# Optimization experiments

Hardware: AMD Instinct MI355X
Metric: run time of the kernel (lower is better)

Reference implementation:

```python
import jax, jax.numpy as jnp
import numpy as np

D = 4  # search range -> 2*D+1 = 9 correlation channels


def setup_inputs() -> dict:
    key = jax.random.key(0)
    k1, k2 = jax.random.split(key)
    N, C, H, W = 4, 128, 192, 640
    feature1 = jax.random.normal(k1, (N, C, H, W), dtype=jnp.float32)
    feature2 = jax.random.normal(k2, (N, C, H, W), dtype=jnp.float32)
    return {"feature1": feature1, "feature2": feature2}


def reference(feature1, feature2):
    # feature1, feature2: [N, C, H, W]
    N, C, H, W = feature1.shape
    d = D
    # Pad feature2 along width: [N, C, H, W + 2d]
    f2p = jnp.pad(feature2, ((0, 0), (0, 0), (0, 0), (d, d)))
    # For each shift i in [0, 2d], correlate feature1 with f2p[..., i:i+W]
    # and take the channel mean -> [N, 1, H, W]; concatenate over shifts.
    costs = [
        jnp.mean(feature1 * jax.lax.dynamic_slice_in_dim(f2p, i, W, axis=3),
                 axis=1, keepdims=True)
        for i in range(2 * d + 1)
    ]
    return jnp.concatenate(costs, axis=1)  # [N, 2d+1, H, W]
```

## Files before the change

### kernel.cpp

```cpp
#include <hip/hip_runtime.h>


constexpr int DD = 4;
constexpr int NSHIFT = 2 * DD + 1;
constexpr int N_ = 4, C_ = 128, H_ = 192, W_ = 640;

__global__ __launch_bounds__(320)
void cost_volume_kernel(const float* __restrict__ f1,
                        const float* __restrict__ f2,
                        float* __restrict__ out)
{
    constexpr int HW = H_ * W_;
    const int t   = threadIdx.x;
    const int row = blockIdx.x;
    const int n   = row / H_;
    const int h   = row - n * H_;

    const float* f1row = f1 + (size_t)n * C_ * HW + (size_t)h * W_;
    const float* f2row = f2 + (size_t)n * C_ * HW + (size_t)h * W_;

    __shared__ float s[2][W_ + 2 * DD];

    if (t < DD) {
        s[0][t] = 0.f;            s[1][t] = 0.f;
        s[0][DD + W_ + t] = 0.f;  s[1][DD + W_ + t] = 0.f;
    }

    const int w = 2 * t;
    float acc0[NSHIFT], acc1[NSHIFT];
#pragma unroll
    for (int i = 0; i < NSHIFT; ++i) { acc0[i] = 0.f; acc1[i] = 0.f; }

    float2 a = *(const float2*)(f1row + w);
    {
        float2 b0 = *(const float2*)(f2row + w);
        *(float2*)&s[0][DD + w] = b0;
    }
    __syncthreads();

    int p = 0;
    for (int c = 0; c < C_ - 1; ++c) {
        const float2 b_n = *(const float2*)(f2row + (size_t)(c + 1) * HW + w);
        const float2 a_n = *(const float2*)(f1row + (size_t)(c + 1) * HW + w);

        float v[NSHIFT + 1];
        const float* sp = &s[p][w];
#pragma unroll
        for (int i = 0; i < 5; ++i)
            *(float2*)&v[2 * i] = *(const float2*)(sp + 2 * i);
#pragma unroll
        for (int i = 0; i < NSHIFT; ++i) {
            acc0[i] = fmaf(a.x, v[i],     acc0[i]);
            acc1[i] = fmaf(a.y, v[i + 1], acc1[i]);
        }

        *(float2*)&s[p ^ 1][DD + w] = b_n;
        __syncthreads();
        a = a_n;
        p ^= 1;
    }

    {
        float v[NSHIFT + 1];
        const float* sp = &s[p][w];
#pragma unroll
        for (int i = 0; i < 5; ++i)
            *(float2*)&v[2 * i] = *(const float2*)(sp + 2 * i);
#pragma unroll
        for (int i = 0; i < NSHIFT; ++i) {
            acc0[i] = fmaf(a.x, v[i],     acc0[i]);
            acc1[i] = fmaf(a.y, v[i + 1], acc1[i]);
        }
    }

    constexpr float scale = 1.0f / (float)C_;
    float* orow = out + (size_t)n * NSHIFT * HW + (size_t)h * W_ + w;
#pragma unroll
    for (int i = 0; i < NSHIFT; ++i) {
        float2 o;
        o.x = acc0[i] * scale;
        o.y = acc1[i] * scale;
        *(float2*)(orow + (size_t)i * HW) = o;
    }
}

extern "C" void kernel_launch(void* const* d_in, const int* in_sizes, int n_in,
                              void* d_out, int out_size, void* d_ws, size_t ws_size,
                              hipStream_t stream) {
    const float* f1 = (const float*)d_in[0];
    const float* f2 = (const float*)d_in[1];
    float* out = (float*)d_out;
    dim3 grid(N_ * H_);
    dim3 block(320);
    cost_volume_kernel<<<grid, block, 0, stream>>>(f1, f2, out);
}
```

Measured before the change: 476.1 us.

## Replace shared-memory staging with direct float4 neighbor loads and register blocking

Removes the shared-memory double buffer and the per-channel __syncthreads. Each thread now loads its own float4 of feature2 plus the float4 on either side straight from global memory, with pointers clamped at the row edges. Out-of-range shift results are masked to zero when writing the output. Each thread covers 4 output columns with 36 accumulators, and a two-channel prefetch pipeline hides load latency. The cost is three times the feature2 load traffic, which relies on the cache, and half as many threads per block, which lowers the number of warps resident per CU.

```diff
diff --git a/kernel.cpp b/kernel.cpp
--- a/kernel.cpp
+++ b/kernel.cpp
@@ -2,85 +2,82 @@
 
 
 constexpr int DD = 4;
-constexpr int NSHIFT = 2 * DD + 1;
+constexpr int NS = 2 * DD + 1;
 constexpr int N_ = 4, C_ = 128, H_ = 192, W_ = 640;
+constexpr int HW = H_ * W_;
 
-__global__ __launch_bounds__(320)
+__device__ __forceinline__ float4 ld4(const float* p) {
+    return *reinterpret_cast<const float4*>(p);
+}
+
+__global__ __launch_bounds__(160)
 void cost_volume_kernel(const float* __restrict__ f1,
                         const float* __restrict__ f2,
                         float* __restrict__ out)
 {
-    constexpr int HW = H_ * W_;
     const int t   = threadIdx.x;
     const int row = blockIdx.x;
     const int n   = row / H_;
     const int h   = row - n * H_;
+    const int w   = 4 * t;
 
-    const float* f1row = f1 + (size_t)n * C_ * HW + (size_t)h * W_;
-    const float* f2row = f2 + (size_t)n * C_ * HW + (size_t)h * W_;
+    const size_t base = (size_t)n * C_ * HW + (size_t)h * W_ + w;
+    const float* pa = f1 + base;
+    const float* p1 = f2 + base;
+    const float* p0 = p1 + (w >= 4 ? -4 : 0);
+    const float* p2 = p1 + (w + 7 < W_ ? 4 : 0);
 
-    __shared__ float s[2][W_ + 2 * DD];
+    float acc[NS][4];
+#pragma unroll
+    for (int i = 0; i < NS; ++i)
+#pragma unroll
+        for (int j = 0; j < 4; ++j) acc[i][j] = 0.f;
 
-    if (t < DD) {
-        s[0][t] = 0.f;            s[1][t] = 0.f;
-        s[0][DD + W_ + t] = 0.f;  s[1][DD + W_ + t] = 0.f;
+#define FMA_STEP(A, U, V, X)                                              \
+    do {                                                                  \
+        float vv[12];                                                     \
+        *(float4*)&vv[0] = (U);                                           \
+        *(float4*)&vv[4] = (V);                                           \
+        *(float4*)&vv[8] = (X);                                           \
+        const float* ap = (const float*)&(A);                             \
+        _Pragma("unroll")                                                 \
+        for (int i = 0; i < NS; ++i) {                                    \
+            _Pragma("unroll")                                             \
+            for (int j = 0; j < 4; ++j)                                   \
+                acc[i][j] = fmaf(ap[j], vv[i + j], acc[i][j]);            \
+        }                                                                 \
+    } while (0)
+
+    float4 a0 = ld4(pa),      u0 = ld4(p0),      v0 = ld4(p1),      x0 = ld4(p2);
+    float4 a1 = ld4(pa + HW), u1 = ld4(p0 + HW), v1 = ld4(p1 + HW), x1 = ld4(p2 + HW);
+    pa += 2 * HW; p0 += 2 * HW; p1 += 2 * HW; p2 += 2 * HW;
+
+    for (int c = 0; c < C_ - 2; c += 2) {
+        float4 ta = ld4(pa), tu = ld4(p0), tv = ld4(p1), tx = ld4(p2);
+        FMA_STEP(a0, u0, v0, x0);
+        a0 = ta; u0 = tu; v0 = tv; x0 = tx;
+        float4 sa = ld4(pa + HW), su = ld4(p0 + HW), sv = ld4(p1 + HW), sx = ld4(p2 + HW);
+        FMA_STEP(a1, u1, v1, x1);
+        a1 = sa; u1 = su; v1 = sv; x1 = sx;
+        pa += 2 * HW; p0 += 2 * HW; p1 += 2 * HW; p2 += 2 * HW;
     }
+    FMA_STEP(a0, u0, v0, x0);
+    FMA_STEP(a1, u1, v1, x1);
 
-    const int w = 2 * t;
-    float acc0[NSHIFT], acc1[NSHIFT];
-#pragma unroll
-    for (int i = 0; i < NSHIFT; ++i) { acc0[i] = 0.f; acc1[i] = 0.f; }
-
-    float2 a = *(const float2*)(f1row + w);
-    {
-        float2 b0 = *(const float2*)(f2row + w);
-        *(float2*)&s[0][DD + w] = b0;
-    }
-    __syncthreads();
-
-    int p = 0;
-    for (int c = 0; c < C_ - 1; ++c) {
-        const float2 b_n = *(const float2*)(f2row + (size_t)(c + 1) * HW + w);
-        const float2 a_n = *(const float2*)(f1row + (size_t)(c + 1) * HW + w);
-
-        float v[NSHIFT + 1];
-        const float* sp = &s[p][w];
-#pragma unroll
-        for (int i = 0; i < 5; ++i)
-            *(float2*)&v[2 * i] = *(const float2*)(sp + 2 * i);
-#pragma unroll
-        for (int i = 0; i < NSHIFT; ++i) {
-            acc0[i] = fmaf(a.x, v[i],     acc0[i]);
-            acc1[i] = fmaf(a.y, v[i + 1], acc1[i]);
-        }
-
-        *(float2*)&s[p ^ 1][DD + w] = b_n;
-        __syncthreads();
-        a = a_n;
-        p ^= 1;
-    }
-
-    {
-        float v[NSHIFT + 1];
-        const float* sp = &s[p][w];
-#pragma unroll
-        for (int i = 0; i < 5; ++i)
-            *(float2*)&v[2 * i] = *(const float2*)(sp + 2 * i);
-#pragma unroll
-        for (int i = 0; i < NSHIFT; ++i) {
-            acc0[i] = fmaf(a.x, v[i],     acc0[i]);
-            acc1[i] = fmaf(a.y, v[i + 1], acc1[i]);
-        }
-    }
+#undef FMA_STEP
 
     constexpr float scale = 1.0f / (float)C_;
-    float* orow = out + (size_t)n * NSHIFT * HW + (size_t)h * W_ + w;
+    float* op = out + (size_t)n * NS * HW + (size_t)h * W_ + w;
 #pragma unroll
-    for (int i = 0; i < NSHIFT; ++i) {
-        float2 o;
-        o.x = acc0[i] * scale;
-        o.y = acc1[i] * scale;
-        *(float2*)(orow + (size_t)i * HW) = o;
+    for (int i = 0; i < NS; ++i) {
+        float4 o;
+        float* oo = (float*)&o;
+#pragma unroll
+        for (int j = 0; j < 4; ++j) {
+            const int idx = w + i + j - DD;
+            oo[j] = (idx >= 0 && idx < W_) ? acc[i][j] * scale : 0.f;
+        }
+        *reinterpret_cast<float4*>(op + (size_t)i * HW) = o;
     }
 }
 
@@ -91,6 +88,6 @@
     const float* f2 = (const float*)d_in[1];
     float* out = (float*)d_out;
     dim3 grid(N_ * H_);
-    dim3 block(320);
+    dim3 block(160);
     cost_volume_kernel<<<grid, block, 0, stream>>>(f1, f2, out);
 }
```

New measurement: 478.4 us. About the same (+0.5%).
